# Optimization experiments

Measured on AMD Instinct MI355X. Metric: run time of the kernel, lower is better.

Reference implementation:

```python
import jax, jax.numpy as jnp
import numpy as np
import math

B, L, X, E, Y = 2, 1024, 4, 128, 4  # batch, win_size/seq, search heads, head dim, retrieval heads


def setup_inputs() -> dict:
    key = jax.random.key(0)
    ks = jax.random.split(key, 12)
    f = jnp.float32
    x = jax.random.normal(ks[0], (B, L, X, E), f)
    query = jax.random.normal(ks[1], (B, L, X, E), f)
    k = jax.random.normal(ks[2], (B, L, X, E), f)
    value = jax.random.normal(ks[3], (B, L, Y, E), f)
    sigma = jax.random.normal(ks[4], (B, L, X), f)
    q_plus = jax.random.normal(ks[5], (B, L, X, E), f)
    # custom triangular mask over (search, retrieval) dims, broadcastable to scores [B,L,M,X,Y]
    attn_mask = jnp.triu(jnp.ones((X, Y), dtype=bool), k=1)
    # Linear(E,E) params (key_plus projection and V projection)
    s = 1.0 / math.sqrt(E)
    Wk = jax.random.normal(ks[6], (E, E), f) * s
    bk = jax.random.normal(ks[7], (E,), f) * s
    Wv = jax.random.normal(ks[8], (E, E), f) * s
    bv = jax.random.normal(ks[9], (E,), f) * s
    return {"x": x, "query": query, "key": k, "value": value, "sigma": sigma,
            "attn_mask": attn_mask, "retrieval": Y, "search": X, "q_plus": q_plus,
            "Wk": Wk, "bk": bk, "Wv": Wv, "bv": bv}


def reference(x, query, key, value, sigma, attn_mask, retrieval, search, q_plus, Wk, bk, Wv, bv):
    Bq, Lq, Hq, Eq = query.shape
    scale = 1.0 / math.sqrt(Eq)
    # stage 1: search attention over keys, per search-head x
    Search = jax.nn.softmax(jnp.einsum('blxe,bsxe->bxls', query, key) * scale, axis=-1)  # [B,X,L,S]
    Retrieval = jnp.einsum('bxls,bsye->blexy', Search, value)  # [B,L,E,X,Y]
    # key_plus = Linear(E,E) over the E axis of Retrieval
    key_plus = jnp.einsum('blexy,fe->blfxy', Retrieval, Wk) + bk[None, None, :, None, None]  # [B,L,E,X,Y]
    # stage 2: scores between q_plus and retrieved keys
    scores = jnp.einsum('blxe,bmexy->blmxy', q_plus, key_plus)  # [B,L,M,X,Y]
    scores = jnp.where(attn_mask[None, None, None, :, :], -jnp.inf, scores)
    series = jax.nn.softmax(scores * scale, axis=-1)  # softmax over Y (retrieval)
    # sigma transform -> Gaussian prior over |i-j| distances
    sig = jnp.transpose(sigma, (0, 2, 1))               # [B,Hs,L]
    sig = jax.nn.sigmoid(sig * 5.0) + 1e-5
    sig = jnp.power(3.0, sig) - 1.0
    sig = sig[..., None]                                # [B,Hs,L,1]
    idx = jnp.arange(Lq, dtype=jnp.float32)
    dist = jnp.abs(idx[:, None] - idx[None, :])         # [L,L]
    prior = 1.0 / (np.float32(math.sqrt(2.0 * math.pi)) * sig) * jnp.exp(-dist ** 2 / 2.0 / sig ** 2)  # [B,Hs,L,L]
    # dropout p=0.0 -> identity
    catt = jnp.einsum('blsxy,bsexy->blexy', series, Retrieval)  # [B,L,E,X,Y]
    V = jnp.sum(catt, axis=-1)                           # chunk over Y then sum -> [B,L,E,X]
    V_list = V.reshape(Bq, Lq, search, -1)               # row-major reinterpret == torch .view
    V = jnp.einsum('blse,fe->blsf', V_list, Wv) + bv     # [B,L,search,E]
    series_out = jnp.mean(jnp.transpose(series, (0, 3, 1, 2, 4)), axis=-1)  # chunk/sum/retrieval == mean over Y -> [B,X,L,M]
    return V, series_out, prior, sig
```

## Files before the change

### kernel.cpp

```cpp
#include <hip/hip_runtime.h>
#include <math.h>

#define B 2
#define L 1024
#define X 4
#define E 128
#define Y 4
#define SCALE 0.08838834764831845f

typedef unsigned short u16;
typedef __attribute__((ext_vector_type(8))) short bf16frag;
typedef __attribute__((ext_vector_type(4))) float floatx4;

static __device__ __forceinline__ u16 bfr(float f) {
  union { float f; unsigned u; } c; c.f = f;
  unsigned r = (c.u + 0x7fffu + ((c.u >> 16) & 1u)) >> 16;
  return (u16)r;
}

__global__ __launch_bounds__(256) void k_prep(const float* __restrict__ q,
                                              const float* __restrict__ key,
                                              const float* __restrict__ value,
                                              const float* __restrict__ sigma,
                                              const float* __restrict__ Wv,
                                              const float* __restrict__ Wk,
                                              float4* __restrict__ sout4,
                                              u16* __restrict__ qkb,
                                              float* __restrict__ colsum,
                                              u16* __restrict__ vt,
                                              float4* __restrict__ wv4t,
                                              u16* __restrict__ wkf,
                                              float* __restrict__ prior,
                                              float* __restrict__ sigout) {
  __shared__ float shp[2];
  const int bid = blockIdx.x;
  const int t = threadIdx.x;
  if (bid < 8192) {
    sout4[bid * 256 + t] = make_float4(0.25f, 0.25f, 0.25f, 0.25f);
  } else if (bid < 8208) {
    const int idx = (bid - 8192) * 256 + t;
    const int e4 = idx >> 7, f = idx & 127;
    wv4t[idx] = *(const float4*)(Wv + f * E + e4 * 4);
  } else if (bid < 9232) {
    if (bid == 8208) colsum[t] = 0.f;
    const int f = (bid - 8208) * 256 + t;
    const int row = f >> 4, c8 = (f & 15) * 8;
    const int sel = row >> 13, row2 = row & 8191;
    const int b = row2 >> 12, l = (row2 >> 2) & 1023, x = row2 & 3;
    const float* src = (sel ? key : q) + (size_t)row2 * E + c8;
    float4 v0 = *(const float4*)src;
    float4 v1 = *(const float4*)(src + 4);
    u16 us[8] = {bfr(v0.x), bfr(v0.y), bfr(v0.z), bfr(v0.w),
                 bfr(v1.x), bfr(v1.y), bfr(v1.z), bfr(v1.w)};
    u16* dst = qkb + (size_t)(sel * 8192 + (b * 4 + x) * 1024 + l) * E + c8;
    *(uint4*)dst = *(uint4*)us;
  } else if (bid < 9360) {
    const int blk = bid - 9232;
    const int by = blk >> 4, sc2 = blk & 15;
    const int b = by >> 2, y = by & 3;
    const int e = t & 127, sh = t >> 7;
    const int s0 = sc2 * 64 + sh * 32;
    u16 us[32];
#pragma unroll 8
    for (int ss = 0; ss < 32; ++ss)
      us[ss] = bfr(value[((size_t)((b * L + s0 + ss) * Y + y)) * E + e]);
    u16* dst = vt + ((size_t)(by * E + e)) * L + s0;
#pragma unroll
    for (int i = 0; i < 4; ++i) *(uint4*)(dst + i * 8) = *(uint4*)&us[i * 8];
  } else if (bid < 17552) {
    const int row = bid - 9360;
    const int bx = row >> 10;
    const int i = row & 1023;
    const int b = bx >> 2, x = bx & 3;
    if (t == 0) {
      const double sv = (double)sigma[((size_t)(b * L + i)) * X + x];
      const double sg = 1.0 / (1.0 + exp(-5.0 * sv)) + 1e-5;
      const double s3 = exp(sg * 1.0986122886681098) - 1.0;
      shp[0] = (float)(1.0 / (2.5066282746310002 * s3));
      shp[1] = (float)(0.5 / (s3 * s3));
      sigout[row] = (float)s3;
    }
    __syncthreads();
    const float coef = shp[0], inv2s2 = shp[1];
    const float di = (float)i;
    const int j0 = t * 4;
    float4 o; float d;
    d = di - (float)(j0 + 0); o.x = coef * __expf(-d * d * inv2s2);
    d = di - (float)(j0 + 1); o.y = coef * __expf(-d * d * inv2s2);
    d = di - (float)(j0 + 2); o.z = coef * __expf(-d * d * inv2s2);
    d = di - (float)(j0 + 3); o.w = coef * __expf(-d * d * inv2s2);
    *(float4*)(prior + (size_t)row * 1024 + j0) = o;
  } else {
    const int idx = (bid - 17552) * 256 + t;
    const int slot = idx >> 6, lane2 = idx & 63;
    const int col = lane2 & 15, quad = lane2 >> 4;
    const int eg = slot >> 4, ft = (slot >> 2) & 3, k = slot & 3;
    const float* src = Wk + (size_t)((eg * 4 + ft) * 16 + col) * E + k * 32 + quad * 8;
    float4 w0 = *(const float4*)src;
    float4 w1 = *(const float4*)(src + 4);
    u16 us[8] = {bfr(w0.x), bfr(w0.y), bfr(w0.z), bfr(w0.w),
                 bfr(w1.x), bfr(w1.y), bfr(w1.z), bfr(w1.w)};
    *(uint4*)(wkf + (size_t)idx * 8) = *(uint4*)us;
  }
}

__global__ __launch_bounds__(512) void k1_mfma(const u16* __restrict__ qb,
                                               const u16* __restrict__ kb,
                                               u16* __restrict__ sbh,
                                               float* __restrict__ isum) {
  __shared__ __align__(16) u16 Qt[16][136];
  __shared__ __align__(16) u16 Kt[128][136];
  __shared__ float red[8][16];
  const int t = threadIdx.x;
  const int blk = blockIdx.x;
  const int lt = blk & 63, bx = blk >> 6;
  const int l0 = lt * 16;
  const int lane = t & 63, w = t >> 6;
  const int col = lane & 15, quad = lane >> 4;
  if (t < 256) {
    const int r = t >> 4, c8 = (t & 15) * 8;
    *(uint4*)&Qt[r][c8] = *(const uint4*)(qb + (size_t)(bx * L + l0 + r) * E + c8);
  }
  __syncthreads();
  bf16frag af[4];
#pragma unroll
  for (int k = 0; k < 4; ++k)
    af[k] = *(const bf16frag*)&Qt[col][k * 32 + quad * 8];

  float rs[4] = {0.f, 0.f, 0.f, 0.f};
  for (int sc = 0; sc < 8; ++sc) {
    __syncthreads();
    {
      const int r = t >> 2, c = (t & 3) * 32;
      const u16* src = kb + (size_t)(bx * L + sc * 128 + r) * E + c;
#pragma unroll
      for (int i = 0; i < 4; ++i)
        *(uint4*)&Kt[r][c + i * 8] = *(const uint4*)(src + i * 8);
    }
    __syncthreads();
    floatx4 acc = (floatx4){0.f, 0.f, 0.f, 0.f};
#pragma unroll
    for (int k = 0; k < 4; ++k) {
      bf16frag bk = *(const bf16frag*)&Kt[w * 16 + col][k * 32 + quad * 8];
      acc = __builtin_amdgcn_mfma_f32_16x16x32_bf16(af[k], bk, acc, 0, 0, 0);
    }
    const size_t so = (size_t)sc * 128 + w * 16 + col;
#pragma unroll
    for (int r = 0; r < 4; ++r) {
      float p = __expf(acc[r] * SCALE);
      rs[r] += p;
      sbh[(size_t)(bx * L + l0 + quad * 4 + r) * L + so] = bfr(p);
    }
  }
#pragma unroll
  for (int m = 1; m <= 8; m <<= 1)
#pragma unroll
    for (int r = 0; r < 4; ++r) rs[r] += __shfl_xor(rs[r], m, 64);
  __syncthreads();
  if (col == 0)
#pragma unroll
    for (int r = 0; r < 4; ++r) red[w][quad * 4 + r] = rs[r];
  __syncthreads();
  if (w == 0 && col == 0)
#pragma unroll
    for (int r = 0; r < 4; ++r) {
      float s = 0.f;
#pragma unroll
      for (int j = 0; j < 8; ++j) s += red[j][quad * 4 + r];
      isum[bx * L + l0 + quad * 4 + r] = 1.0f / s;
    }
}

__global__ __launch_bounds__(256) void k34_retr_kp(const u16* __restrict__ sbh,
                                                   const u16* __restrict__ vt,
                                                   const float* __restrict__ isum,
                                                   const u16* __restrict__ wkf,
                                                   const float* __restrict__ bk,
                                                   u16* __restrict__ kp_bf,
                                                   u16* __restrict__ rt_bf,
                                                   float* __restrict__ colsum) {
  __shared__ __align__(16) unsigned char smem[23040];
  u16 (*Pt)[72] = (u16(*)[72])smem;
  u16 (*Vt)[72] = (u16(*)[72])(smem + 4608);
  float (*Rt)[132] = (float(*)[132])smem;
  const int t = threadIdx.x;
  const int blk = (blockIdx.x & 7) * 80 + (blockIdx.x >> 3);
  const int lt = blk & 31;
  const int cp = blk >> 5;
  const int b = cp / 10, p = cp % 10;
  const int x = (p >= 6) ? 3 : (p >= 3) ? 2 : (p >= 1) ? 1 : 0;
  const int y = p - ((x * (x + 1)) >> 1);
  const int by = b * 4 + y;
  const int srow = (b * 4 + x) * L;
  const int l0 = lt * 32;
  const int lane = t & 63, w = t >> 6;
  const int col = lane & 15, quad = lane >> 4;
  const int lw = w >> 1, eg = w & 1;
  floatx4 vf[4];
#pragma unroll
  for (int i = 0; i < 4; ++i) vf[i] = (floatx4){0.f, 0.f, 0.f, 0.f};
  for (int sc2 = 0; sc2 < 16; ++sc2) {
    const int s0 = sc2 * 64;
    __syncthreads();
    {
      const int r = t >> 3, c8 = (t & 7) * 8;
      *(uint4*)&Pt[r][c8] = *(const uint4*)(sbh + (size_t)(srow + l0 + r) * L + s0 + c8);
    }
    {
      const int e = t >> 1, off = (t & 1) * 32;
      const u16* src = vt + ((size_t)(by * E + e)) * L + s0 + off;
#pragma unroll
      for (int i = 0; i < 4; ++i)
        *(uint4*)&Vt[e][off + i * 8] = *(const uint4*)(src + i * 8);
    }
    __syncthreads();
#pragma unroll
    for (int ks = 0; ks < 2; ++ks) {
      bf16frag pf = *(const bf16frag*)&Pt[lw * 16 + col][ks * 32 + quad * 8];
#pragma unroll
      for (int i = 0; i < 4; ++i) {
        bf16frag rf = *(const bf16frag*)&Vt[(eg * 4 + i) * 16 + col][ks * 32 + quad * 8];
        vf[i] = __builtin_amdgcn_mfma_f32_16x16x32_bf16(pf, rf, vf[i], 0, 0, 0);
      }
    }
  }
  float is[4];
#pragma unroll
  for (int r = 0; r < 4; ++r) is[r] = isum[srow + l0 + lw * 16 + quad * 4 + r];
  __syncthreads();
#pragma unroll
  for (int i = 0; i < 4; ++i)
#pragma unroll
    for (int r = 0; r < 4; ++r)
      Rt[lw * 16 + quad * 4 + r][(eg * 4 + i) * 16 + col] = vf[i][r] * is[r];
  __syncthreads();
  if (p == 0) {
    if (t < 128) {
      float ssum = 0.f;
#pragma unroll
      for (int r = 0; r < 32; ++r) ssum += Rt[r][t];
      atomicAdd(&colsum[b * 128 + t], ssum);
    }
    return;
  }
  const int cslot = b * 9 + (p - 1);
  bf16frag aR[4];
#pragma unroll
  for (int k = 0; k < 4; ++k) {
    u16 us[8];
#pragma unroll
    for (int j = 0; j < 8; ++j) us[j] = bfr(Rt[lw * 16 + col][k * 32 + quad * 8 + j]);
    aR[k] = *(bf16frag*)us;
  }
#pragma unroll
  for (int ft = 0; ft < 4; ++ft) {
    const int f0 = (eg * 4 + ft) * 16;
    floatx4 c = (floatx4){0.f, 0.f, 0.f, 0.f};
#pragma unroll
    for (int k = 0; k < 4; ++k) {
      bf16frag bf = *(const bf16frag*)&wkf[(size_t)((((eg * 4 + ft) * 4 + k) * 64) + lane) * 8];
      c = __builtin_amdgcn_mfma_f32_16x16x32_bf16(aR[k], bf, c, 0, 0, 0);
    }
    const float bias = bk[f0 + col];
#pragma unroll
    for (int r = 0; r < 4; ++r)
      kp_bf[((size_t)(cslot * L + l0 + lw * 16 + quad * 4 + r)) * E + f0 + col] =
          bfr(c[r] + bias);
  }
  {
    const int e = t >> 1, half = t & 1;
    u16 us[16];
#pragma unroll
    for (int j = 0; j < 16; ++j) us[j] = bfr(Rt[half * 16 + j][e]);
    u16* dst = rt_bf + ((size_t)(cslot * E + e)) * L + l0 + half * 16;
    *(uint4*)dst = *(uint4*)&us[0];
    *(uint4*)(dst + 8) = *(uint4*)&us[8];
  }
}

template<int NY>
static __device__ __forceinline__ void k5_body(const float* __restrict__ qp,
                                               const u16* __restrict__ kp_bf,
                                               const u16* __restrict__ rt_bf,
                                               float* __restrict__ vws,
                                               u16 (*__restrict__ uni)[128][40],
                                               u16 (*__restrict__ pT)[32][40],
                                               const int t, const int b,
                                               const int lt, const int part,
                                               const int slotbase) {
  constexpr int x = NY - 1;
  u16 (*kpT)[32][136] = (u16 (*)[32][136])uni;
  const int mc0 = part * 4;
  const int l0 = lt * 32;
  const int lane = t & 63, w = t >> 6;
  const int col = lane & 15, quad = lane >> 4;
  const int lw = w >> 1, mt = w & 1, eg = w & 1;
  const int smr = t >> 3, se0 = (t & 7) * 16;
  const int sre = t >> 1, srh = (t & 1) * 16;

  bf16frag af[4];
  {
    const float* qpr = qp + ((size_t)((b * L + l0 + lw * 16 + col) * X + x)) * E;
#pragma unroll
    for (int k = 0; k < 4; ++k) {
      float4 v0 = *(const float4*)(qpr + k * 32 + quad * 8);
      float4 v1 = *(const float4*)(qpr + k * 32 + quad * 8 + 4);
      u16 us[8] = {bfr(v0.x), bfr(v0.y), bfr(v0.z), bfr(v0.w),
                   bfr(v1.x), bfr(v1.y), bfr(v1.z), bfr(v1.w)};
      af[k] = *(bf16frag*)us;
    }
  }
  floatx4 vf[4];
#pragma unroll
  for (int i = 0; i < 4; ++i) vf[i] = (floatx4){0.f, 0.f, 0.f, 0.f};

  for (int mc = mc0; mc < mc0 + 4; ++mc) {
    const int m0 = mc * 32;
    __syncthreads();
#pragma unroll
    for (int y = 0; y < NY; ++y) {
      const u16* src = kp_bf + ((size_t)(slotbase + y) * L + m0 + smr) * E + se0;
      uint4 a0 = *(const uint4*)src;
      uint4 a1 = *(const uint4*)(src + 8);
      *(uint4*)&kpT[y][smr][se0] = a0;
      *(uint4*)&kpT[y][smr][se0 + 8] = a1;
    }
    __syncthreads();
    floatx4 sf[NY];
#pragma unroll
    for (int y = 0; y < NY; ++y) sf[y] = (floatx4){0.f, 0.f, 0.f, 0.f};
#pragma unroll
    for (int y = 0; y < NY; ++y)
#pragma unroll
      for (int k = 0; k < 4; ++k) {
        bf16frag bkf = *(const bf16frag*)&kpT[y][mt * 16 + col][k * 32 + quad * 8];
        sf[y] = __builtin_amdgcn_mfma_f32_16x16x32_bf16(af[k], bkf, sf[y], 0, 0, 0);
      }
    u16 pu[NY][4];
#pragma unroll
    for (int r = 0; r < 4; ++r) {
      float zz[NY]; float mx = -3.4e38f;
#pragma unroll
      for (int y = 0; y < NY; ++y) { zz[y] = sf[y][r] * SCALE; mx = fmaxf(mx, zz[y]); }
      float sum = 0.f;
#pragma unroll
      for (int y = 0; y < NY; ++y) { zz[y] = __expf(zz[y] - mx); sum += zz[y]; }
      float inv = 1.0f / sum;
#pragma unroll
      for (int y = 0; y < NY; ++y) pu[y][r] = bfr(zz[y] * inv);
    }
    __syncthreads();
#pragma unroll
    for (int y = 0; y < NY; ++y) {
#pragma unroll
      for (int r = 0; r < 4; ++r)
        pT[y][lw * 16 + quad * 4 + r][mt * 16 + col] = pu[y][r];
      const u16* src = rt_bf + ((size_t)(slotbase + y) * E + sre) * L + m0 + srh;
      uint4 a0 = *(const uint4*)src;
      uint4 a1 = *(const uint4*)(src + 8);
      *(uint4*)&uni[y][sre][srh] = a0;
      *(uint4*)&uni[y][sre][srh + 8] = a1;
    }
    __syncthreads();
#pragma unroll
    for (int y = 0; y < NY; ++y) {
      bf16frag pf = *(const bf16frag*)&pT[y][lw * 16 + col][quad * 8];
#pragma unroll
      for (int i = 0; i < 4; ++i) {
        bf16frag rf = *(const bf16frag*)&uni[y][(eg * 4 + i) * 16 + col][quad * 8];
        vf[i] = __builtin_amdgcn_mfma_f32_16x16x32_bf16(pf, rf, vf[i], 0, 0, 0);
      }
    }
  }
  float* dst = vws + (size_t)(b * 24 + (x - 1) * 8 + part) * (L * E) + (size_t)l0 * E;
#pragma unroll
  for (int i = 0; i < 4; ++i)
#pragma unroll
    for (int r = 0; r < 4; ++r)
      dst[((size_t)(lw * 16 + quad * 4 + r)) * E + (eg * 4 + i) * 16 + col] = vf[i][r];
}

__global__ __launch_bounds__(256) void k5_stage2(const float* __restrict__ qp,
                                                 const u16* __restrict__ kp_bf,
                                                 const u16* __restrict__ rt_bf,
                                                 float* __restrict__ vws) {
  __shared__ __align__(16) u16 uni[4][128][40];
  __shared__ __align__(16) u16 pT[4][32][40];
  const int t = threadIdx.x;
  const int vb = (blockIdx.x & 7) * 192 + (blockIdx.x >> 3);
  const int g = vb >> 8;
  const int r = vb & 255;
  const int b = g / 3, xm1 = g % 3;
  const int part = r >> 5, lt = r & 31;
  const int slotbase = b * 9 + ((xm1 == 0) ? 0 : (xm1 == 1) ? 2 : 5);
  if (xm1 == 0)      k5_body<2>(qp, kp_bf, rt_bf, vws, uni, pT, t, b, lt, part, slotbase);
  else if (xm1 == 1) k5_body<3>(qp, kp_bf, rt_bf, vws, uni, pT, t, b, lt, part, slotbase);
  else               k5_body<4>(qp, kp_bf, rt_bf, vws, uni, pT, t, b, lt, part, slotbase);
}

__global__ __launch_bounds__(256) void k6_vout(const float* __restrict__ vws,
                                               const float4* __restrict__ wv4t,
                                               const float* __restrict__ bv,
                                               const float* __restrict__ colsum,
                                               float* __restrict__ vout) {
  __shared__ __align__(16) float rowf[8][512];
  const int t = threadIdx.x;
  const int blk = blockIdx.x;
  const int bl0 = blk * 8;
  const int b = bl0 >> 10;
  const int lbase = bl0 & 1023;
  {
    const int o = t * 2;
    const int xh = o >> 7, e = o & 127;
    if (xh == 0) {
      const float sx = colsum[b * 128 + e];
      const float sy = colsum[b * 128 + e + 1];
#pragma unroll
      for (int l8 = 0; l8 < 8; ++l8) {
        rowf[l8][e * 4] = sx;
        rowf[l8][(e + 1) * 4] = sy;
      }
    } else {
      const size_t pbase = (size_t)(b * 24 + (xh - 1) * 8) * 131072;
#pragma unroll
      for (int l8 = 0; l8 < 8; ++l8) {
        const size_t base = pbase + (size_t)(lbase + l8) * 128 + e;
        float sx = 0.f, sy = 0.f;
#pragma unroll
        for (int p = 0; p < 8; ++p) {
          float2 v = *(const float2*)(vws + base + (size_t)p * 131072);
          sx += v.x; sy += v.y;
        }
        rowf[l8][e * 4 + xh] = sx;
        rowf[l8][(e + 1) * 4 + xh] = sy;
      }
    }
  }
  __syncthreads();
#pragma unroll
  for (int rep = 0; rep < 2; ++rep) {
    const int o = t + rep * 256;
    const int s = o >> 7, f = o & 127;
    float acc[8] = {0.f, 0.f, 0.f, 0.f, 0.f, 0.f, 0.f, 0.f};
    const float4* wp = wv4t + f;
#pragma unroll 4
    for (int e4 = 0; e4 < 32; ++e4) {
      const float4 wv = wp[e4 * 128];
#pragma unroll
      for (int l8 = 0; l8 < 8; ++l8) {
        const float4 rv = *(const float4*)&rowf[l8][(s * 32 + e4) * 4];
        acc[l8] += wv.x * rv.x + wv.y * rv.y + wv.z * rv.z + wv.w * rv.w;
      }
    }
    const float bb = bv[f];
#pragma unroll
    for (int l8 = 0; l8 < 8; ++l8)
      vout[(size_t)(bl0 + l8) * 512 + s * 128 + f] = acc[l8] + bb;
  }
}

extern "C" void kernel_launch(void* const* d_in, const int* in_sizes, int n_in,
                              void* d_out, int out_size, void* d_ws, size_t ws_size,
                              hipStream_t stream) {
  const float* q     = (const float*)d_in[1];
  const float* key   = (const float*)d_in[2];
  const float* value = (const float*)d_in[3];
  const float* sigma = (const float*)d_in[4];
  const float* qp    = (const float*)d_in[8];
  const float* Wk    = (const float*)d_in[9];
  const float* bk    = (const float*)d_in[10];
  const float* Wv    = (const float*)d_in[11];
  const float* bv    = (const float*)d_in[12];

  float* out    = (float*)d_out;
  float* Vout   = out;
  float* sout   = out + 1048576;
  float* prior  = out + 9437184;
  float* sigout = out + 17825792;

  float* ws     = (float*)d_ws;
  u16*   sbh    = (u16*)ws;
  u16*   qb     = (u16*)(ws + 4194304);
  u16*   kb     = qb + 1048576;
  u16*   vt     = (u16*)(ws + 5242880);
  float* isum   = ws + 5767168;
  float* wv4t   = ws + 6291456;
  u16*   wkf    = (u16*)(ws + 6307840);
  u16*   kp_bf  = (u16*)(ws + 8388608);
  u16*   rt_bf  = (u16*)(ws + 9568256);
  float* colsum = ws + 10747904;
  float* vws    = ws;

  hipLaunchKernelGGL(k_prep,      dim3(17560), dim3(256), 0, stream, q, key, value, sigma,
                     Wv, Wk, (float4*)sout, (u16*)qb, colsum, vt, (float4*)wv4t, wkf, prior, sigout);
  hipLaunchKernelGGL(k1_mfma,     dim3(512),  dim3(512), 0, stream, qb, kb, sbh, isum);
  hipLaunchKernelGGL(k34_retr_kp, dim3(640),  dim3(256), 0, stream, sbh, vt, isum, wkf, bk, kp_bf, rt_bf, colsum);
  hipLaunchKernelGGL(k5_stage2,   dim3(1536), dim3(256), 0, stream, qp, kp_bf, rt_bf, vws);
  hipLaunchKernelGGL(k6_vout,     dim3(256),  dim3(256), 0, stream, vws, (const float4*)wv4t, bv, colsum, Vout);
}
```

Measured before the change: 203.6 us.

## Fuse search-softmax score kernel into retrieval kernel, recomputing QK^T per block

Merges the QK^T/exp kernel into the retrieval-plus-key-projection kernel. Each block now computes the unnormalized softmax tile from Q and K on the fly, stages it in shared memory and feeds it straight into the P·V MFMA. The row-sum reciprocal is reduced inside the block. This removes the bf16 score matrix write and read through global memory, plus one launch. In exchange, QK^T is recomputed for each (x,y) pair sharing the same x, and shared memory use and the number of syncs per iteration grow.

```diff
diff --git a/kernel.cpp b/kernel.cpp
--- a/kernel.cpp
+++ b/kernel.cpp
@@ -104,84 +104,20 @@
   }
 }
 
-__global__ __launch_bounds__(512) void k1_mfma(const u16* __restrict__ qb,
-                                               const u16* __restrict__ kb,
-                                               u16* __restrict__ sbh,
-                                               float* __restrict__ isum) {
-  __shared__ __align__(16) u16 Qt[16][136];
-  __shared__ __align__(16) u16 Kt[128][136];
-  __shared__ float red[8][16];
-  const int t = threadIdx.x;
-  const int blk = blockIdx.x;
-  const int lt = blk & 63, bx = blk >> 6;
-  const int l0 = lt * 16;
-  const int lane = t & 63, w = t >> 6;
-  const int col = lane & 15, quad = lane >> 4;
-  if (t < 256) {
-    const int r = t >> 4, c8 = (t & 15) * 8;
-    *(uint4*)&Qt[r][c8] = *(const uint4*)(qb + (size_t)(bx * L + l0 + r) * E + c8);
-  }
-  __syncthreads();
-  bf16frag af[4];
-#pragma unroll
-  for (int k = 0; k < 4; ++k)
-    af[k] = *(const bf16frag*)&Qt[col][k * 32 + quad * 8];
-
-  float rs[4] = {0.f, 0.f, 0.f, 0.f};
-  for (int sc = 0; sc < 8; ++sc) {
-    __syncthreads();
-    {
-      const int r = t >> 2, c = (t & 3) * 32;
-      const u16* src = kb + (size_t)(bx * L + sc * 128 + r) * E + c;
-#pragma unroll
-      for (int i = 0; i < 4; ++i)
-        *(uint4*)&Kt[r][c + i * 8] = *(const uint4*)(src + i * 8);
-    }
-    __syncthreads();
-    floatx4 acc = (floatx4){0.f, 0.f, 0.f, 0.f};
-#pragma unroll
-    for (int k = 0; k < 4; ++k) {
-      bf16frag bk = *(const bf16frag*)&Kt[w * 16 + col][k * 32 + quad * 8];
-      acc = __builtin_amdgcn_mfma_f32_16x16x32_bf16(af[k], bk, acc, 0, 0, 0);
-    }
-    const size_t so = (size_t)sc * 128 + w * 16 + col;
-#pragma unroll
-    for (int r = 0; r < 4; ++r) {
-      float p = __expf(acc[r] * SCALE);
-      rs[r] += p;
-      sbh[(size_t)(bx * L + l0 + quad * 4 + r) * L + so] = bfr(p);
-    }
-  }
-#pragma unroll
-  for (int m = 1; m <= 8; m <<= 1)
-#pragma unroll
-    for (int r = 0; r < 4; ++r) rs[r] += __shfl_xor(rs[r], m, 64);
-  __syncthreads();
-  if (col == 0)
-#pragma unroll
-    for (int r = 0; r < 4; ++r) red[w][quad * 4 + r] = rs[r];
-  __syncthreads();
-  if (w == 0 && col == 0)
-#pragma unroll
-    for (int r = 0; r < 4; ++r) {
-      float s = 0.f;
-#pragma unroll
-      for (int j = 0; j < 8; ++j) s += red[j][quad * 4 + r];
-      isum[bx * L + l0 + quad * 4 + r] = 1.0f / s;
-    }
-}
-
-__global__ __launch_bounds__(256) void k34_retr_kp(const u16* __restrict__ sbh,
-                                                   const u16* __restrict__ vt,
-                                                   const float* __restrict__ isum,
-                                                   const u16* __restrict__ wkf,
-                                                   const float* __restrict__ bk,
-                                                   u16* __restrict__ kp_bf,
-                                                   u16* __restrict__ rt_bf,
-                                                   float* __restrict__ colsum) {
-  __shared__ __align__(16) unsigned char smem[23040];
-  u16 (*Pt)[72] = (u16(*)[72])smem;
-  u16 (*Vt)[72] = (u16(*)[72])(smem + 4608);
+__global__ __launch_bounds__(256) void k134_fused(const u16* __restrict__ qb,
+                                                  const u16* __restrict__ kb,
+                                                  const u16* __restrict__ vt,
+                                                  const u16* __restrict__ wkf,
+                                                  const float* __restrict__ bk,
+                                                  u16* __restrict__ kp_bf,
+                                                  u16* __restrict__ rt_bf,
+                                                  float* __restrict__ colsum) {
+  __shared__ __align__(16) unsigned char smem[40832];
+  u16 (*Kt)[136] = (u16(*)[136])smem;
+  u16 (*Vt)[72]  = (u16(*)[72])(smem + 17408);
+  u16 (*pT)[72]  = (u16(*)[72])(smem + 35840);
+  float* red     = (float*)(smem + 40448);
+  float* inv_l   = (float*)(smem + 40704);
   float (*Rt)[132] = (float(*)[132])smem;
   const int t = threadIdx.x;
   const int blk = (blockIdx.x & 7) * 80 + (blockIdx.x >> 3);
@@ -190,21 +126,32 @@
   const int b = cp / 10, p = cp % 10;
   const int x = (p >= 6) ? 3 : (p >= 3) ? 2 : (p >= 1) ? 1 : 0;
   const int y = p - ((x * (x + 1)) >> 1);
+  const int bx = b * 4 + x;
   const int by = b * 4 + y;
-  const int srow = (b * 4 + x) * L;
   const int l0 = lt * 32;
   const int lane = t & 63, w = t >> 6;
   const int col = lane & 15, quad = lane >> 4;
-  const int lw = w >> 1, eg = w & 1;
+  const int lw = w >> 1, mt = w & 1, eg = w & 1;
+
+  bf16frag af[4];
+#pragma unroll
+  for (int k = 0; k < 4; ++k)
+    af[k] = *(const bf16frag*)(qb + (size_t)(bx * L + l0 + lw * 16 + col) * E + k * 32 + quad * 8);
+
   floatx4 vf[4];
 #pragma unroll
   for (int i = 0; i < 4; ++i) vf[i] = (floatx4){0.f, 0.f, 0.f, 0.f};
-  for (int sc2 = 0; sc2 < 16; ++sc2) {
-    const int s0 = sc2 * 64;
+  float rs[4] = {0.f, 0.f, 0.f, 0.f};
+
+  for (int sc = 0; sc < 16; ++sc) {
+    const int s0 = sc * 64;
     __syncthreads();
     {
-      const int r = t >> 3, c8 = (t & 7) * 8;
-      *(uint4*)&Pt[r][c8] = *(const uint4*)(sbh + (size_t)(srow + l0 + r) * L + s0 + c8);
+      const int r = t >> 2, c = (t & 3) * 32;
+      const u16* src = kb + (size_t)(bx * L + s0 + r) * E + c;
+#pragma unroll
+      for (int i = 0; i < 4; ++i)
+        *(uint4*)&Kt[r][c + i * 8] = *(const uint4*)(src + i * 8);
     }
     {
       const int e = t >> 1, off = (t & 1) * 32;
@@ -216,7 +163,23 @@
     __syncthreads();
 #pragma unroll
     for (int ks = 0; ks < 2; ++ks) {
-      bf16frag pf = *(const bf16frag*)&Pt[lw * 16 + col][ks * 32 + quad * 8];
+      floatx4 sf = (floatx4){0.f, 0.f, 0.f, 0.f};
+#pragma unroll
+      for (int k = 0; k < 4; ++k) {
+        bf16frag bkf = *(const bf16frag*)&Kt[ks * 32 + mt * 16 + col][k * 32 + quad * 8];
+        sf = __builtin_amdgcn_mfma_f32_16x16x32_bf16(af[k], bkf, sf, 0, 0, 0);
+      }
+#pragma unroll
+      for (int r = 0; r < 4; ++r) {
+        float pexp = __expf(sf[r] * SCALE);
+        rs[r] += pexp;
+        pT[lw * 16 + quad * 4 + r][ks * 32 + mt * 16 + col] = bfr(pexp);
+      }
+    }
+    __syncthreads();
+#pragma unroll
+    for (int ks = 0; ks < 2; ++ks) {
+      bf16frag pf = *(const bf16frag*)&pT[lw * 16 + col][ks * 32 + quad * 8];
 #pragma unroll
       for (int i = 0; i < 4; ++i) {
         bf16frag rf = *(const bf16frag*)&Vt[(eg * 4 + i) * 16 + col][ks * 32 + quad * 8];
@@ -224,10 +187,25 @@
       }
     }
   }
+#pragma unroll
+  for (int m = 1; m <= 8; m <<= 1)
+#pragma unroll
+    for (int r = 0; r < 4; ++r) rs[r] += __shfl_xor(rs[r], m, 64);
+  __syncthreads();
+  if (col == 0)
+#pragma unroll
+    for (int r = 0; r < 4; ++r) red[w * 16 + quad * 4 + r] = rs[r];
+  __syncthreads();
+  if (mt == 0 && col == 0)
+#pragma unroll
+    for (int r = 0; r < 4; ++r) {
+      const float s = red[(lw * 2) * 16 + quad * 4 + r] + red[(lw * 2 + 1) * 16 + quad * 4 + r];
+      inv_l[lw * 16 + quad * 4 + r] = 1.0f / s;
+    }
+  __syncthreads();
   float is[4];
 #pragma unroll
-  for (int r = 0; r < 4; ++r) is[r] = isum[srow + l0 + lw * 16 + quad * 4 + r];
-  __syncthreads();
+  for (int r = 0; r < 4; ++r) is[r] = inv_l[lw * 16 + quad * 4 + r];
 #pragma unroll
   for (int i = 0; i < 4; ++i)
 #pragma unroll
@@ -479,11 +457,9 @@
   float* sigout = out + 17825792;
 
   float* ws     = (float*)d_ws;
-  u16*   sbh    = (u16*)ws;
   u16*   qb     = (u16*)(ws + 4194304);
   u16*   kb     = qb + 1048576;
   u16*   vt     = (u16*)(ws + 5242880);
-  float* isum   = ws + 5767168;
   float* wv4t   = ws + 6291456;
   u16*   wkf    = (u16*)(ws + 6307840);
   u16*   kp_bf  = (u16*)(ws + 8388608);
@@ -491,10 +467,9 @@
   float* colsum = ws + 10747904;
   float* vws    = ws;
 
-  hipLaunchKernelGGL(k_prep,      dim3(17560), dim3(256), 0, stream, q, key, value, sigma,
+  hipLaunchKernelGGL(k_prep,     dim3(17560), dim3(256), 0, stream, q, key, value, sigma,
                      Wv, Wk, (float4*)sout, (u16*)qb, colsum, vt, (float4*)wv4t, wkf, prior, sigout);
-  hipLaunchKernelGGL(k1_mfma,     dim3(512),  dim3(512), 0, stream, qb, kb, sbh, isum);
-  hipLaunchKernelGGL(k34_retr_kp, dim3(640),  dim3(256), 0, stream, sbh, vt, isum, wkf, bk, kp_bf, rt_bf, colsum);
-  hipLaunchKernelGGL(k5_stage2,   dim3(1536), dim3(256), 0, stream, qp, kp_bf, rt_bf, vws);
-  hipLaunchKernelGGL(k6_vout,     dim3(256),  dim3(256), 0, stream, vws, (const float4*)wv4t, bv, colsum, Vout);
-}
+  hipLaunchKernelGGL(k134_fused, dim3(640),  dim3(256), 0, stream, qb, kb, vt, wkf, bk, kp_bf, rt_bf, colsum);
+  hipLaunchKernelGGL(k5_stage2,  dim3(1536), dim3(256), 0, stream, qp, kp_bf, rt_bf, vws);
+  hipLaunchKernelGGL(k6_vout,    dim3(256),  dim3(256), 0, stream, vws, (const float4*)wv4t, bv, colsum, Vout);
+}
```

Measured after the change: 214.1 us. 1.05x slower.
